# Optimization experiments

Hardware: AMD Instinct MI355X
Metric: run time of the kernel (lower is better)

Reference implementation:

```python
import jax, jax.numpy as jnp
from jax import lax
import numpy as np

B, T, F, H = 64, 512, 256, 512


def _gru_scan(data_tbf, Wi, bi, Wh, bhn):
    """Run a flax-style GRUCell over time. data_tbf: (T, B, F) -> (T, B, H)."""
    def step(h, x):
        xg = x @ Wi + bi              # (B, 3H): ir | iz | in
        hg = h @ Wh                   # (B, 3H): hr | hz | hn (hn bias added below)
        xr, xz, xn = jnp.split(xg, 3, axis=-1)
        hr, hz, hn = jnp.split(hg, 3, axis=-1)
        r = jax.nn.sigmoid(xr + hr)
        z = jax.nn.sigmoid(xz + hz)
        n = jnp.tanh(xn + r * (hn + bhn))
        new_h = (1.0 - z) * n + z * h
        return new_h, new_h

    h0 = jnp.zeros((data_tbf.shape[1], Wh.shape[0]), data_tbf.dtype)
    _, ys = lax.scan(step, h0, data_tbf)
    return ys


def setup_inputs() -> dict:
    key = jax.random.key(0)
    ks = jax.random.split(key, 5)
    s_i = 1.0 / np.sqrt(F)
    s_h = 1.0 / np.sqrt(H)
    return {
        "data": jax.random.normal(ks[0], (B, T, F), jnp.float32),
        "Wi_f": jax.random.normal(ks[1], (F, 3 * H), jnp.float32) * s_i,
        "bi_f": jnp.zeros((3 * H,), jnp.float32),
        "Wh_f": jax.random.normal(ks[2], (H, 3 * H), jnp.float32) * s_h,
        "bhn_f": jnp.zeros((H,), jnp.float32),
        "Wi_b": jax.random.normal(ks[3], (F, 3 * H), jnp.float32) * s_i,
        "bi_b": jnp.zeros((3 * H,), jnp.float32),
        "Wh_b": jax.random.normal(ks[4], (H, 3 * H), jnp.float32) * s_h,
        "bhn_b": jnp.zeros((H,), jnp.float32),
    }


def reference(data, Wi_f, bi_f, Wh_f, bhn_f, Wi_b, bi_b, Wh_b, bhn_b):
    # Forward direction: scan over time (axis 1 of data)
    fwd = _gru_scan(jnp.swapaxes(data, 0, 1), Wi_f, bi_f, Wh_f, bhn_f)
    fwd = jnp.swapaxes(fwd, 0, 1)                      # (B, T, H)
    # 'Backward' direction: source flips axis 0 (batch), faithfully reproduced.
    rev = jnp.flip(data, axis=0)
    bwd = _gru_scan(jnp.swapaxes(rev, 0, 1), Wi_b, bi_b, Wh_b, bhn_b)
    bwd = jnp.swapaxes(bwd, 0, 1)                      # (B, T, H)
    bwd = jnp.flip(bwd, axis=0)
    return jnp.concatenate([fwd, bwd], axis=-1)        # (B, T, 2H)
```

## Files before the change

### kernel.cpp

```cpp
#include <hip/hip_runtime.h>
#include <hip/hip_bf16.h>


#define BB 64
#define TT 512
#define FF 256
#define HH 512
#define G3 1536
#define NSLICE 32
#define NUNIT 8
#define NWG (NSLICE * NUNIT)
#define NTHR 192

typedef __attribute__((ext_vector_type(8))) short short8;
typedef __attribute__((ext_vector_type(4))) float f32x4;

__device__ __forceinline__ unsigned short f2bf(float f) {
  union { float f; unsigned u; } x; x.f = f;
  unsigned r = (x.u + 0x7fffu + ((x.u >> 16) & 1u)) >> 16;
  return (unsigned short)r;
}

__global__ __launch_bounds__(NTHR) void gru_fused(
    const float* __restrict__ data,
    const float* __restrict__ Wi_f, const float* __restrict__ bi_f,
    const float* __restrict__ Wh_f, const float* __restrict__ bhn_f,
    const float* __restrict__ Wi_b, const float* __restrict__ bi_b,
    const float* __restrict__ Wh_b, const float* __restrict__ bhn_b,
    float* __restrict__ out,
    unsigned long long* __restrict__ hbuf,
    int* __restrict__ flags)
{
  const int wg   = blockIdx.x;
  const int unit = wg & 7;
  const int s    = wg >> 3;
  const int dir  = unit >> 2;
  const int bg   = unit & 3;
  const int tid  = threadIdx.x;
  const int wv   = tid >> 6;
  const int lane = tid & 63;
  const int l15  = lane & 15;
  const int lg   = lane >> 4;

  const float* Wi  = dir ? Wi_b  : Wi_f;
  const float* Wh  = dir ? Wh_b  : Wh_f;
  const float* bi  = dir ? bi_b  : bi_f;
  const float* bhn = dir ? bhn_b : bhn_f;

  __shared__ __align__(16) char hA[16 * 1024];
  __shared__ float hP[16][17];
  __shared__ float r_s[16][17];
  __shared__ float z_s[16][17];

  const int colT = s * 16 + l15;
  const int gcol = wv * HH + colT;

  short8 whf[16];
#pragma unroll
  for (int ks = 0; ks < 16; ++ks) {
    short8 v;
#pragma unroll
    for (int j = 0; j < 8; ++j) v[j] = (short)f2bf(Wh[(ks * 32 + lg * 8 + j) * G3 + gcol]);
    whf[ks] = v;
  }
  short8 wif[8];
#pragma unroll
  for (int ks = 0; ks < 8; ++ks) {
    short8 v;
#pragma unroll
    for (int j = 0; j < 8; ++j) v[j] = (short)f2bf(Wi[(ks * 32 + lg * 8 + j) * G3 + gcol]);
    wif[ks] = v;
  }
  const float bic  = bi[gcol];
  const float bhnc = bhn[colT];

  int* myflags = flags + unit * TT;
  const float* xbase = data + (size_t)(bg * 16 + l15) * TT * FF;
  const int sw = (l15 & 7) << 4;

  for (int t = 0; t < TT; ++t) {
    const int ib = t & 1, ob = ib ^ 1;

    f32x4 accX = {0.f, 0.f, 0.f, 0.f};
    {
      const float* xrow = xbase + t * FF;
#pragma unroll
      for (int ks = 0; ks < 8; ++ks) {
        short8 a;
#pragma unroll
        for (int j = 0; j < 8; ++j) a[j] = (short)f2bf(xrow[ks * 32 + lg * 8 + j]);
        accX = __builtin_amdgcn_mfma_f32_16x16x32_bf16(a, wif[ks], accX, 0, 0, 0);
      }
    }

    if (t > 0 && tid == 0) {
      while (__hip_atomic_load(&myflags[t - 1], __ATOMIC_RELAXED, __HIP_MEMORY_SCOPE_AGENT) < NSLICE) {
        __builtin_amdgcn_s_sleep(1);
      }
    }
    __syncthreads();

    {
      const unsigned long long* hin = hbuf + (size_t)(dir * 2 + ib) * 512 * 32;
      for (int i = tid; i < 4096; i += NTHR) {
        int col = i >> 3;
        int pr  = i & 7;
        unsigned long long v = __hip_atomic_load(
            (unsigned long long*)(hin + (size_t)col * 32 + bg * 8 + pr),
            __ATOMIC_RELAXED, __HIP_MEMORY_SCOPE_AGENT);
        union { unsigned u; float f; } lo, hi;
        lo.u = (unsigned)v; hi.u = (unsigned)(v >> 32);
        int r0 = pr * 2, r1 = r0 + 1;
        *(unsigned short*)(hA + r0 * 1024 + ((col * 2) ^ ((r0 & 7) << 4))) = f2bf(lo.f);
        *(unsigned short*)(hA + r1 * 1024 + ((col * 2) ^ ((r1 & 7) << 4))) = f2bf(hi.f);
        if ((col >> 4) == s) { hP[r0][col & 15] = lo.f; hP[r1][col & 15] = hi.f; }
      }
    }
    __syncthreads();

    f32x4 accH = {0.f, 0.f, 0.f, 0.f};
    {
      const char* arow = hA + l15 * 1024;
#pragma unroll
      for (int ks = 0; ks < 16; ++ks) {
        short8 a = *(const short8*)(arow + ((ks * 64 + lg * 16) ^ sw));
        accH = __builtin_amdgcn_mfma_f32_16x16x32_bf16(a, whf[ks], accH, 0, 0, 0);
      }
    }

    if (wv == 0) {
#pragma unroll
      for (int j = 0; j < 4; ++j) {
        float pre = accX[j] + accH[j] + bic;
        r_s[lg * 4 + j][l15] = 1.f / (1.f + __expf(-pre));
      }
    } else if (wv == 1) {
#pragma unroll
      for (int j = 0; j < 4; ++j) {
        float pre = accX[j] + accH[j] + bic;
        z_s[lg * 4 + j][l15] = 1.f / (1.f + __expf(-pre));
      }
    }
    __syncthreads();

    if (wv == 2) {
      float hv[4];
#pragma unroll
      for (int j = 0; j < 4; ++j) {
        int row = lg * 4 + j;
        float r  = r_s[row][l15];
        float z  = z_s[row][l15];
        float hp = hP[row][l15];
        float n  = tanhf(accX[j] + bic + r * (accH[j] + bhnc));
        hv[j] = (1.f - z) * n + z * hp;
        out[((size_t)(bg * 16 + row) * TT + t) * 1024 + dir * 512 + colT] = hv[j];
      }
      union { float f; unsigned u; } c0, c1, c2, c3;
      c0.f = hv[0]; c1.f = hv[1]; c2.f = hv[2]; c3.f = hv[3];
      unsigned long long p0 = (unsigned long long)c0.u | ((unsigned long long)c1.u << 32);
      unsigned long long p1 = (unsigned long long)c2.u | ((unsigned long long)c3.u << 32);
      unsigned long long* hout = hbuf + (size_t)(dir * 2 + ob) * 512 * 32;
      size_t bidx = (size_t)colT * 32 + bg * 8 + lg * 2;
      __hip_atomic_store(&hout[bidx],     p0, __ATOMIC_RELAXED, __HIP_MEMORY_SCOPE_AGENT);
      __hip_atomic_store(&hout[bidx + 1], p1, __ATOMIC_RELAXED, __HIP_MEMORY_SCOPE_AGENT);
      asm volatile("s_waitcnt vmcnt(0)" ::: "memory");
      if (lane == 0)
        __hip_atomic_fetch_add(&myflags[t], 1, __ATOMIC_RELAXED, __HIP_MEMORY_SCOPE_AGENT);
    }
  }
}

extern "C" void kernel_launch(void* const* d_in, const int* in_sizes, int n_in,
                              void* d_out, int out_size, void* d_ws, size_t ws_size,
                              hipStream_t stream) {
  const float* data  = (const float*)d_in[0];
  const float* Wi_f  = (const float*)d_in[1];
  const float* bi_f  = (const float*)d_in[2];
  const float* Wh_f  = (const float*)d_in[3];
  const float* bhn_f = (const float*)d_in[4];
  const float* Wi_b  = (const float*)d_in[5];
  const float* bi_b  = (const float*)d_in[6];
  const float* Wh_b  = (const float*)d_in[7];
  const float* bhn_b = (const float*)d_in[8];
  float* out = (float*)d_out;

  unsigned long long* hbuf = (unsigned long long*)d_ws;
  int* flags = (int*)((char*)d_ws + 524288);
  hipMemsetAsync(d_ws, 0, 524288 + 16384, stream);

  gru_fused<<<NWG, NTHR, 0, stream>>>(data, Wi_f, bi_f, Wh_f, bhn_f,
                                      Wi_b, bi_b, Wh_b, bhn_b, out, hbuf, flags);
}
```

Before: 4.464 ms.

## Collapse GRU workgroup to one wave holding all three gates' weights in registers

Each workgroup becomes a single 64-lane wave that computes the r, z and n gate MFMAs itself, with all weights held in registers. This removes the shared-memory gate exchange and the __syncthreads barriers on the serial per-timestep critical path. The hidden-state exchange buffer now stores bf16 in the MFMA A-operand layout, so the wave loads fragments straight from global memory instead of converting and staging through LDS. The register footprint roughly triples, and sigmoid/tanh use fast rcp/exp approximations, which slightly reduces precision.

```diff
diff --git a/kernel.cpp b/kernel.cpp
--- a/kernel.cpp
+++ b/kernel.cpp
@@ -2,26 +2,35 @@
 #include <hip/hip_bf16.h>
 
 
-#define BB 64
 #define TT 512
 #define FF 256
 #define HH 512
 #define G3 1536
 #define NSLICE 32
-#define NUNIT 8
-#define NWG (NSLICE * NUNIT)
-#define NTHR 192
+#define NWG 256
+#define NTHR 64
 
 typedef __attribute__((ext_vector_type(8))) short short8;
 typedef __attribute__((ext_vector_type(4))) float f32x4;
 
 __device__ __forceinline__ unsigned short f2bf(float f) {
   union { float f; unsigned u; } x; x.f = f;
-  unsigned r = (x.u + 0x7fffu + ((x.u >> 16) & 1u)) >> 16;
-  return (unsigned short)r;
+  return (unsigned short)((x.u + 0x7fffu + ((x.u >> 16) & 1u)) >> 16);
 }
 
-__global__ __launch_bounds__(NTHR) void gru_fused(
+__device__ __forceinline__ unsigned pk2(float a, float b) {
+  union { __hip_bfloat162 h; unsigned u; } x;
+  x.h = __float22bfloat162_rn(make_float2(a, b));
+  return x.u;
+}
+
+__device__ __forceinline__ float sigm(float x) {
+  return __builtin_amdgcn_rcpf(1.f + __expf(-x));
+}
+
+#define MFMA(a, b, c) __builtin_amdgcn_mfma_f32_16x16x32_bf16((a), (b), (c), 0, 0, 0)
+
+__global__ __launch_bounds__(NTHR, 1) void gru_fused(
     const float* __restrict__ data,
     const float* __restrict__ Wi_f, const float* __restrict__ bi_f,
     const float* __restrict__ Wh_f, const float* __restrict__ bhn_f,
@@ -36,9 +45,7 @@
   const int s    = wg >> 3;
   const int dir  = unit >> 2;
   const int bg   = unit & 3;
-  const int tid  = threadIdx.x;
-  const int wv   = tid >> 6;
-  const int lane = tid & 63;
+  const int lane = threadIdx.x;
   const int l15  = lane & 15;
   const int lg   = lane >> 4;
 
@@ -47,126 +54,110 @@
   const float* bi  = dir ? bi_b  : bi_f;
   const float* bhn = dir ? bhn_b : bhn_f;
 
-  __shared__ __align__(16) char hA[16 * 1024];
-  __shared__ float hP[16][17];
-  __shared__ float r_s[16][17];
-  __shared__ float z_s[16][17];
+  const int colT = s * 16 + l15;
 
-  const int colT = s * 16 + l15;
-  const int gcol = wv * HH + colT;
-
-  short8 whf[16];
+  short8 whf[3][16];
 #pragma unroll
-  for (int ks = 0; ks < 16; ++ks) {
-    short8 v;
+  for (int g = 0; g < 3; ++g)
 #pragma unroll
-    for (int j = 0; j < 8; ++j) v[j] = (short)f2bf(Wh[(ks * 32 + lg * 8 + j) * G3 + gcol]);
-    whf[ks] = v;
-  }
-  short8 wif[8];
+    for (int ks = 0; ks < 16; ++ks) {
+      short8 v;
 #pragma unroll
-  for (int ks = 0; ks < 8; ++ks) {
-    short8 v;
+      for (int j = 0; j < 8; ++j)
+        v[j] = (short)f2bf(Wh[(size_t)(ks * 32 + lg * 8 + j) * G3 + g * HH + colT]);
+      whf[g][ks] = v;
+    }
+  short8 wif[3][8];
 #pragma unroll
-    for (int j = 0; j < 8; ++j) v[j] = (short)f2bf(Wi[(ks * 32 + lg * 8 + j) * G3 + gcol]);
-    wif[ks] = v;
-  }
-  const float bic  = bi[gcol];
+  for (int g = 0; g < 3; ++g)
+#pragma unroll
+    for (int ks = 0; ks < 8; ++ks) {
+      short8 v;
+#pragma unroll
+      for (int j = 0; j < 8; ++j)
+        v[j] = (short)f2bf(Wi[(size_t)(ks * 32 + lg * 8 + j) * G3 + g * HH + colT]);
+      wif[g][ks] = v;
+    }
+  const float biR = bi[colT], biZ = bi[HH + colT], biN = bi[2 * HH + colT];
   const float bhnc = bhn[colT];
 
   int* myflags = flags + unit * TT;
   const float* xbase = data + (size_t)(bg * 16 + l15) * TT * FF;
-  const int sw = (l15 & 7) << 4;
+
+  __shared__ __align__(16) unsigned short tile[16][16];
+
+  float hp[4] = {0.f, 0.f, 0.f, 0.f};
 
   for (int t = 0; t < TT; ++t) {
-    const int ib = t & 1, ob = ib ^ 1;
+    const int ib = t & 1;
 
-    f32x4 accX = {0.f, 0.f, 0.f, 0.f};
+    f32x4 accR = {0.f, 0.f, 0.f, 0.f};
+    f32x4 accZ = {0.f, 0.f, 0.f, 0.f};
+    f32x4 xN   = {0.f, 0.f, 0.f, 0.f};
     {
-      const float* xrow = xbase + t * FF;
+      const float* xr = xbase + (size_t)t * FF;
 #pragma unroll
       for (int ks = 0; ks < 8; ++ks) {
-        short8 a;
-#pragma unroll
-        for (int j = 0; j < 8; ++j) a[j] = (short)f2bf(xrow[ks * 32 + lg * 8 + j]);
-        accX = __builtin_amdgcn_mfma_f32_16x16x32_bf16(a, wif[ks], accX, 0, 0, 0);
+        float4 x0 = *(const float4*)(xr + ks * 32 + lg * 8);
+        float4 x1 = *(const float4*)(xr + ks * 32 + lg * 8 + 4);
+        union { short8 s; unsigned u[4]; } a;
+        a.u[0] = pk2(x0.x, x0.y); a.u[1] = pk2(x0.z, x0.w);
+        a.u[2] = pk2(x1.x, x1.y); a.u[3] = pk2(x1.z, x1.w);
+        accR = MFMA(a.s, wif[0][ks], accR);
+        accZ = MFMA(a.s, wif[1][ks], accZ);
+        xN   = MFMA(a.s, wif[2][ks], xN);
       }
     }
 
-    if (t > 0 && tid == 0) {
-      while (__hip_atomic_load(&myflags[t - 1], __ATOMIC_RELAXED, __HIP_MEMORY_SCOPE_AGENT) < NSLICE) {
+    if (t > 0) {
+      while (__hip_atomic_load(&myflags[t - 1], __ATOMIC_RELAXED, __HIP_MEMORY_SCOPE_AGENT) < NSLICE)
         __builtin_amdgcn_s_sleep(1);
-      }
-    }
-    __syncthreads();
-
-    {
-      const unsigned long long* hin = hbuf + (size_t)(dir * 2 + ib) * 512 * 32;
-      for (int i = tid; i < 4096; i += NTHR) {
-        int col = i >> 3;
-        int pr  = i & 7;
-        unsigned long long v = __hip_atomic_load(
-            (unsigned long long*)(hin + (size_t)col * 32 + bg * 8 + pr),
-            __ATOMIC_RELAXED, __HIP_MEMORY_SCOPE_AGENT);
-        union { unsigned u; float f; } lo, hi;
-        lo.u = (unsigned)v; hi.u = (unsigned)(v >> 32);
-        int r0 = pr * 2, r1 = r0 + 1;
-        *(unsigned short*)(hA + r0 * 1024 + ((col * 2) ^ ((r0 & 7) << 4))) = f2bf(lo.f);
-        *(unsigned short*)(hA + r1 * 1024 + ((col * 2) ^ ((r1 & 7) << 4))) = f2bf(hi.f);
-        if ((col >> 4) == s) { hP[r0][col & 15] = lo.f; hP[r1][col & 15] = hi.f; }
-      }
-    }
-    __syncthreads();
-
-    f32x4 accH = {0.f, 0.f, 0.f, 0.f};
-    {
-      const char* arow = hA + l15 * 1024;
-#pragma unroll
-      for (int ks = 0; ks < 16; ++ks) {
-        short8 a = *(const short8*)(arow + ((ks * 64 + lg * 16) ^ sw));
-        accH = __builtin_amdgcn_mfma_f32_16x16x32_bf16(a, whf[ks], accH, 0, 0, 0);
-      }
+      __builtin_amdgcn_fence(__ATOMIC_ACQUIRE, "agent");
     }
 
-    if (wv == 0) {
+    const unsigned long long* hin = hbuf + (size_t)(unit * 2 + ib) * 2048;
+    unsigned long long q[32];
 #pragma unroll
-      for (int j = 0; j < 4; ++j) {
-        float pre = accX[j] + accH[j] + bic;
-        r_s[lg * 4 + j][l15] = 1.f / (1.f + __expf(-pre));
-      }
-    } else if (wv == 1) {
+    for (int ks = 0; ks < 16; ++ks) {
+      const int bidx = l15 * 128 + ks * 8 + lg * 2;
+      q[2 * ks]     = __hip_atomic_load(&hin[bidx],     __ATOMIC_RELAXED, __HIP_MEMORY_SCOPE_AGENT);
+      q[2 * ks + 1] = __hip_atomic_load(&hin[bidx + 1], __ATOMIC_RELAXED, __HIP_MEMORY_SCOPE_AGENT);
+    }
+
+    f32x4 hN = {0.f, 0.f, 0.f, 0.f};
 #pragma unroll
-      for (int j = 0; j < 4; ++j) {
-        float pre = accX[j] + accH[j] + bic;
-        z_s[lg * 4 + j][l15] = 1.f / (1.f + __expf(-pre));
-      }
+    for (int ks = 0; ks < 16; ++ks) {
+      union { short8 s; unsigned long long q[2]; } a;
+      a.q[0] = q[2 * ks]; a.q[1] = q[2 * ks + 1];
+      accR = MFMA(a.s, whf[0][ks], accR);
+      accZ = MFMA(a.s, whf[1][ks], accZ);
+      hN   = MFMA(a.s, whf[2][ks], hN);
     }
-    __syncthreads();
 
-    if (wv == 2) {
-      float hv[4];
+    float hv[4];
 #pragma unroll
-      for (int j = 0; j < 4; ++j) {
-        int row = lg * 4 + j;
-        float r  = r_s[row][l15];
-        float z  = z_s[row][l15];
-        float hp = hP[row][l15];
-        float n  = tanhf(accX[j] + bic + r * (accH[j] + bhnc));
-        hv[j] = (1.f - z) * n + z * hp;
-        out[((size_t)(bg * 16 + row) * TT + t) * 1024 + dir * 512 + colT] = hv[j];
-      }
-      union { float f; unsigned u; } c0, c1, c2, c3;
-      c0.f = hv[0]; c1.f = hv[1]; c2.f = hv[2]; c3.f = hv[3];
-      unsigned long long p0 = (unsigned long long)c0.u | ((unsigned long long)c1.u << 32);
-      unsigned long long p1 = (unsigned long long)c2.u | ((unsigned long long)c3.u << 32);
-      unsigned long long* hout = hbuf + (size_t)(dir * 2 + ob) * 512 * 32;
-      size_t bidx = (size_t)colT * 32 + bg * 8 + lg * 2;
-      __hip_atomic_store(&hout[bidx],     p0, __ATOMIC_RELAXED, __HIP_MEMORY_SCOPE_AGENT);
-      __hip_atomic_store(&hout[bidx + 1], p1, __ATOMIC_RELAXED, __HIP_MEMORY_SCOPE_AGENT);
-      asm volatile("s_waitcnt vmcnt(0)" ::: "memory");
-      if (lane == 0)
-        __hip_atomic_fetch_add(&myflags[t], 1, __ATOMIC_RELAXED, __HIP_MEMORY_SCOPE_AGENT);
+    for (int j = 0; j < 4; ++j) {
+      float r = sigm(accR[j] + biR);
+      float z = sigm(accZ[j] + biZ);
+      float e = __expf(2.f * (xN[j] + biN + r * (hN[j] + bhnc)));
+      float n = 1.f - 2.f * __builtin_amdgcn_rcpf(e + 1.f);
+      hv[j] = (1.f - z) * n + z * hp[j];
+      hp[j] = hv[j];
     }
+
+#pragma unroll
+    for (int j = 0; j < 4; ++j) tile[lg * 4 + j][l15] = f2bf(hv[j]);
+    unsigned long long pv = *(const unsigned long long*)&tile[l15][lg * 4];
+    unsigned long long* hout = hbuf + (size_t)(unit * 2 + (ib ^ 1)) * 2048;
+    __hip_atomic_store(&hout[l15 * 128 + s * 4 + lg], pv,
+                       __ATOMIC_RELAXED, __HIP_MEMORY_SCOPE_AGENT);
+    asm volatile("s_waitcnt vmcnt(0)" ::: "memory");
+    if (lane == 0)
+      __hip_atomic_fetch_add(&myflags[t], 1, __ATOMIC_RELAXED, __HIP_MEMORY_SCOPE_AGENT);
+
+#pragma unroll
+    for (int j = 0; j < 4; ++j)
+      out[((size_t)(bg * 16 + lg * 4 + j) * TT + t) * 1024 + (size_t)dir * HH + colT] = hv[j];
   }
 }
 
@@ -185,8 +176,8 @@
   float* out = (float*)d_out;
 
   unsigned long long* hbuf = (unsigned long long*)d_ws;
-  int* flags = (int*)((char*)d_ws + 524288);
-  hipMemsetAsync(d_ws, 0, 524288 + 16384, stream);
+  int* flags = (int*)((char*)d_ws + 262144);
+  hipMemsetAsync(d_ws, 0, 262144 + 16384, stream);
 
   gru_fused<<<NWG, NTHR, 0, stream>>>(data, Wi_f, bi_f, Wh_f, bhn_f,
                                       Wi_b, bi_b, Wh_b, bhn_b, out, hbuf, flags);
```

Result: slower. 4.609 ms (+3.2%).
